# Performance work log

Hardware: AMD Instinct MI355X
Metric: run time of the kernel (lower is better)

The kernel has to match this reference:

```python
import jax, jax.numpy as jnp
import numpy as np

HEADS = 8
DIM_HEAD = 64
DIM = 512
INNER = HEADS * DIM_HEAD  # 512
SCALE = DIM_HEAD ** -0.5


def setup_inputs() -> dict:
    key = jax.random.key(0)
    k1, k2, k3, k4 = jax.random.split(key, 4)
    B, N = 2, 4096
    x = jax.random.normal(k1, (B, N, DIM), dtype=jnp.float32)
    # nn.Linear(dim, inner*3, bias=False): weight [3*inner, dim]; y = x @ W.T
    w_qkv = jax.random.normal(k2, (3 * INNER, DIM), dtype=jnp.float32) * (DIM ** -0.5)
    w_out = jax.random.normal(k3, (DIM, INNER), dtype=jnp.float32) * (INNER ** -0.5)
    b_out = jax.random.normal(k4, (DIM,), dtype=jnp.float32) * 0.01
    return {"x": x, "w_qkv": w_qkv, "w_out": w_out, "b_out": b_out, "H": 64, "W": 64}


def reference(x, w_qkv, w_out, b_out, H, W):
    B, N, _ = x.shape
    qkv = jnp.einsum('bnd,ed->bne', x, w_qkv)  # [B, N, 3*inner]
    q, k, v = jnp.split(qkv, 3, axis=-1)
    def to_heads(t):
        return t.reshape(B, N, HEADS, DIM_HEAD).transpose(0, 2, 1, 3)  # b h n d
    q, k, v = to_heads(q), to_heads(k), to_heads(v)
    dots = jnp.einsum('bhid,bhjd->bhij', q, k) * SCALE
    attn = jax.nn.softmax(dots, axis=-1)  # dropout p=0.0 -> identity
    out = jnp.einsum('bhij,bhjd->bhid', attn, v)
    out = out.transpose(0, 2, 1, 3).reshape(B, N, INNER)
    return jnp.einsum('bne,de->bnd', out, w_out) + b_out
```

## Files before the change

### kernel.cpp

```cpp
#include <hip/hip_runtime.h>
#include <hip/hip_bf16.h>

typedef __hip_bfloat16 bf16;
typedef __attribute__((ext_vector_type(8))) short short8;
typedef __attribute__((ext_vector_type(4))) short shortx4;
typedef __attribute__((ext_vector_type(4))) float floatx4;
typedef __attribute__((ext_vector_type(4))) int intx4;

#define MFMA16(a, b, c) __builtin_amdgcn_mfma_f32_16x16x32_bf16((a), (b), (c), 0, 0, 0)
#define EXP2(x) __builtin_amdgcn_exp2f(x)

__device__ __forceinline__ short f2s(float v) {
    return __builtin_bit_cast(short, __float2bfloat16(v));
}

__device__ __forceinline__ int packhi(float lo, float hi) {
    return (int)__builtin_amdgcn_perm(__builtin_bit_cast(unsigned, hi),
                                      __builtin_bit_cast(unsigned, lo),
                                      0x07060302u);
}

__device__ __forceinline__ short8 cvt8v(float4 f0, float4 f1) {
    short8 r;
    r[0] = f2s(f0.x); r[1] = f2s(f0.y); r[2] = f2s(f0.z); r[3] = f2s(f0.w);
    r[4] = f2s(f1.x); r[5] = f2s(f1.y); r[6] = f2s(f1.z); r[7] = f2s(f1.w);
    return r;
}

__device__ __forceinline__ int swz(int row, int chunk) {
    return row * 64 + ((chunk ^ (row & 7)) << 3);
}
__device__ __forceinline__ int swzv(int row, int chunk) {
    return row * 128 + ((chunk ^ (row & 7)) << 3);
}

__global__ __launch_bounds__(256) void cvt_inputs(
    const float* __restrict__ x, const float* __restrict__ wq,
    const float* __restrict__ wo, bf16* __restrict__ xb,
    bf16* __restrict__ wqb, bf16* __restrict__ wob)
{
    int idx = blockIdx.x * 256 + threadIdx.x;
    const float* src;
    bf16* dst;
    int off;
    if (idx < 524288)      { src = x;  dst = xb;  off = idx; }
    else if (idx < 622592) { src = wq; dst = wqb; off = idx - 524288; }
    else                   { src = wo; dst = wob; off = idx - 622592; }
    float4 f0 = ((const float4*)src)[off * 2];
    float4 f1 = ((const float4*)src)[off * 2 + 1];
    *(short8*)&((short*)dst)[off * 8] = cvt8v(f0, f1);
}

__global__ __launch_bounds__(256) void qkv_gemm(
    const bf16* __restrict__ xb, const bf16* __restrict__ wqb,
    bf16* __restrict__ q, bf16* __restrict__ k, bf16* __restrict__ vt)
{
    __shared__ short pool[20480];
    short (*As)[128][40] = (short(*)[128][40])pool;
    short (*Bs)[128][40] = (short(*)[128][40])(pool + 10240);
    short (*Qt)[144] = (short(*)[144])pool;
    short (*Vt)[136] = (short(*)[136])pool;
    const int t = threadIdx.x;
    const int bm = blockIdx.x * 128;
    const int be = blockIdx.y * 128;
    const int w = t >> 6, lane = t & 63, lq = lane >> 4, lm = lane & 15;
    const int wr = w >> 1, wc = w & 1;
    const int srow = t >> 1, scol = (t & 1) * 16;
    const float C = 0.18033688011112042f;

    const bf16* xp = &xb[(size_t)(bm + srow) * 512 + scol];
    const bf16* wp = &wqb[(size_t)(be + srow) * 512 + scol];

    intx4 xr[2], wr4[2];
    auto issue = [&](int k0) {
        xr[0] = *(const intx4*)(xp + k0);
        xr[1] = *(const intx4*)(xp + k0 + 8);
        wr4[0] = *(const intx4*)(wp + k0);
        wr4[1] = *(const intx4*)(wp + k0 + 8);
    };
    auto commit = [&](int buf) {
        *(intx4*)&As[buf][srow][scol]     = xr[0];
        *(intx4*)&As[buf][srow][scol + 8] = xr[1];
        *(intx4*)&Bs[buf][srow][scol]     = wr4[0];
        *(intx4*)&Bs[buf][srow][scol + 8] = wr4[1];
    };

    floatx4 acc[4][4];
#pragma unroll
    for (int i = 0; i < 4; ++i)
#pragma unroll
        for (int j = 0; j < 4; ++j) acc[i][j] = {0.f, 0.f, 0.f, 0.f};

    issue(0);
    commit(0);
    __syncthreads();
    int cur = 0;
    for (int k0 = 0; k0 < 512; k0 += 32) {
        const bool more = (k0 + 32) < 512;
        if (more) issue(k0 + 32);
        short8 af[4], bf[4];
#pragma unroll
        for (int mt = 0; mt < 4; ++mt) af[mt] = *(const short8*)&As[cur][wr * 64 + mt * 16 + lm][lq * 8];
#pragma unroll
        for (int nt = 0; nt < 4; ++nt) bf[nt] = *(const short8*)&Bs[cur][wc * 64 + nt * 16 + lm][lq * 8];
#pragma unroll
        for (int mt = 0; mt < 4; ++mt)
#pragma unroll
            for (int nt = 0; nt < 4; ++nt)
                acc[mt][nt] = MFMA16(af[mt], bf[nt], acc[mt][nt]);
        if (more) {
            commit(cur ^ 1);
            __syncthreads();
        }
        cur ^= 1;
    }

    const int which = be >> 9;
    __syncthreads();
    if (which < 2) {
        const float scale = (which == 0) ? C : 1.0f;
#pragma unroll
        for (int nt = 0; nt < 4; ++nt) {
            const int e_loc = wc * 64 + nt * 16 + lm;
#pragma unroll
            for (int mt = 0; mt < 4; ++mt)
#pragma unroll
                for (int r = 0; r < 4; ++r)
                    Qt[wr * 64 + mt * 16 + lq * 4 + r][e_loc] = f2s(acc[mt][nt][r] * scale);
        }
        __syncthreads();
        bf16* dst = (which == 0) ? q : k;
        const int tr = t >> 1, th = t & 1;
        const int grow = bm + tr;
        const int b = grow >> 12, n = grow & 4095;
        const int h = ((be + th * 64) & 511) >> 6;
        bf16* p = dst + ((size_t)(b * 8 + h) * 4096 + n) * 64;
#pragma unroll
        for (int c = 0; c < 8; ++c)
            *(intx4*)&p[c * 8] = *(const intx4*)&Qt[tr][th * 64 + c * 8];
    } else {
#pragma unroll
        for (int nt = 0; nt < 4; ++nt) {
            const int e_loc = wc * 64 + nt * 16 + lm;
#pragma unroll
            for (int mt = 0; mt < 4; ++mt) {
                const int col = wr * 64 + 4 * (mt & 1) + 8 * lq + 32 * (mt >> 1);
                shortx4 v4;
#pragma unroll
                for (int r = 0; r < 4; ++r) v4[r] = f2s(acc[mt][nt][r]);
                *(shortx4*)&Vt[e_loc][col] = v4;
            }
        }
        __syncthreads();
        const int b = bm >> 12, n0 = bm & 4095;
        const int h0 = (be - 1024) >> 6;
        const int row = t >> 1, cb = (t & 1) * 64;
        const int h = h0 + (row >> 6), d = row & 63;
        const size_t gb = ((size_t)(b * 8 + h) * 64 + d) * 4096 + n0 + cb;
#pragma unroll
        for (int c = 0; c < 8; ++c)
            *(intx4*)&vt[gb + c * 8] = *(const intx4*)&Vt[row][cb + c * 8];
    }
}

__global__ __launch_bounds__(256, 2) void flash_attn(
    const bf16* __restrict__ q, const bf16* __restrict__ k,
    const bf16* __restrict__ vt, bf16* __restrict__ out)
{
    __shared__ short pool[40960];
    short* Qs  = pool;
    short* Ks0 = pool + 8192;
    short* Vs0 = pool + 24576;
    const int t = threadIdx.x;
    const int n = blockIdx.x;
    const int L = (n & 7) * 64 + (n >> 3);
    const int i0 = (L & 31) * 128;
    const int bh = L >> 5;
    const int w = t >> 6, lane = t & 63, lq = lane >> 4, lm = lane & 15;
    const int h = w >> 1;
    const int par = w & 1;
    const floatx4 zero4 = {0.f, 0.f, 0.f, 0.f};

    const size_t nbase = (size_t)bh * 4096 * 64;
    const size_t vbase = (size_t)bh * 64 * 4096;
    const int r0 = t >> 3, ch = t & 7;

#pragma unroll
    for (int it = 0; it < 4; ++it) {
        int row = it * 32 + r0;
        *(intx4*)&Qs[swz(row, ch)] =
            *(const intx4*)&q[nbase + (size_t)(i0 + row) * 64 + ch * 8];
    }

    const int kr = t >> 1, kc = (t & 1) * 4;
    const int vr = t >> 2, vc = (t & 3) * 4;
    const bf16* kp0 = &k[nbase + (size_t)kr * 64 + kc * 8];
    const bf16* vp0 = &vt[vbase + (size_t)vr * 4096 + vc * 8];
    int kso[4], vso[4];
#pragma unroll
    for (int c = 0; c < 4; ++c) {
        kso[c] = swz(kr, kc + c);
        vso[c] = swzv(vr, vc + c);
    }

    intx4 kreg[4], vreg[4];
    auto issue = [&](int j0n) {
        const intx4* kp = (const intx4*)(kp0 + (size_t)j0n * 64);
        const intx4* vp = (const intx4*)(vp0 + j0n);
#pragma unroll
        for (int c = 0; c < 4; ++c) { kreg[c] = kp[c]; vreg[c] = vp[c]; }
    };
    auto commit = [&](int buf) {
        short* Kb = Ks0 + buf * 8192;
        short* Vb = Vs0 + buf * 8192;
#pragma unroll
        for (int c = 0; c < 4; ++c) {
            *(intx4*)&Kb[kso[c]] = kreg[c];
            *(intx4*)&Vb[vso[c]] = vreg[c];
        }
    };

    issue(0);
    commit(0);
    __syncthreads();

    short8 aq0[4], aq1[4];
#pragma unroll
    for (int g = 0; g < 4; ++g) {
        const int qrow = h * 64 + g * 16 + lm;
        aq0[g] = *(const short8*)&Qs[swz(qrow, lq)];
        aq1[g] = *(const short8*)&Qs[swz(qrow, 4 + lq)];
    }

    float l_lane[4] = {0.f, 0.f, 0.f, 0.f};
    floatx4 o_acc[4][4];
#pragma unroll
    for (int g = 0; g < 4; ++g)
#pragma unroll
        for (int dt = 0; dt < 4; ++dt) o_acc[g][dt] = zero4;

    const int jtb = par * 4;
    int cur = 0;
    for (int j0 = 0; j0 < 4096; j0 += 128) {
        const bool more = (j0 + 128) < 4096;
        if (more) issue(j0 + 128);
        const short* Kb = Ks0 + cur * 8192;
        const short* Vb = Vs0 + cur * 8192;

        intx4 pkA[4], pkB[4];
#pragma unroll
        for (int q2 = 0; q2 < 4; ++q2) {
            const int krow = (jtb + q2) * 16 + lm;
            short8 bk0 = *(const short8*)&Kb[swz(krow, lq)];
            short8 bk1 = *(const short8*)&Kb[swz(krow, 4 + lq)];
#pragma unroll
            for (int g = 0; g < 4; ++g) {
                floatx4 s4 = MFMA16(bk0, aq0[g], zero4);
                s4 = MFMA16(bk1, aq1[g], s4);
                float e0 = EXP2(s4[0]);
                float e1 = EXP2(s4[1]);
                float e2 = EXP2(s4[2]);
                float e3 = EXP2(s4[3]);
                l_lane[g] += (e0 + e1) + (e2 + e3);
                int p01 = packhi(e0, e1), p23 = packhi(e2, e3);
                if (q2 < 2) { pkA[g][q2 * 2] = p01; pkA[g][q2 * 2 + 1] = p23; }
                else { pkB[g][(q2 - 2) * 2] = p01; pkB[g][(q2 - 2) * 2 + 1] = p23; }
            }
        }

        __builtin_amdgcn_s_setprio(1);
#pragma unroll
        for (int dt = 0; dt < 4; ++dt) {
            const int vrow = dt * 16 + lm;
            short8 av0 = *(const short8*)&Vb[swzv(vrow, par * 8 + lq)];
            short8 av1 = *(const short8*)&Vb[swzv(vrow, par * 8 + 4 + lq)];
#pragma unroll
            for (int g = 0; g < 4; ++g) {
                o_acc[g][dt] = MFMA16(av0, __builtin_bit_cast(short8, pkA[g]), o_acc[g][dt]);
                o_acc[g][dt] = MFMA16(av1, __builtin_bit_cast(short8, pkB[g]), o_acc[g][dt]);
            }
        }
        __builtin_amdgcn_s_setprio(0);

        if (more) {
            commit(cur ^ 1);
            __syncthreads();
        }
        cur ^= 1;
    }

    __syncthreads();
    float* Red = (float*)(pool + 8192);
    float* Lx  = (float*)pool;
    if (par == 1) {
#pragma unroll
        for (int g = 0; g < 4; ++g) {
            Lx[h * 256 + g * 64 + lane] = l_lane[g];
#pragma unroll
            for (int dt = 0; dt < 4; ++dt)
#pragma unroll
                for (int r = 0; r < 4; ++r)
                    Red[h * 4096 + ((g * 4 + dt) * 4 + r) * 64 + lane] = o_acc[g][dt][r];
        }
    }
    __syncthreads();
    if (par == 0) {
        const int b = bh >> 3, hd = bh & 7;
        short* Os = pool + 1024 + h * 1024;
        const int il = lane >> 2, cc = (lane & 3) * 16;
#pragma unroll
        for (int g = 0; g < 4; ++g) {
            float l = l_lane[g] + Lx[h * 256 + g * 64 + lane];
#pragma unroll
            for (int dt = 0; dt < 4; ++dt)
#pragma unroll
                for (int r = 0; r < 4; ++r)
                    o_acc[g][dt][r] += Red[h * 4096 + ((g * 4 + dt) * 4 + r) * 64 + lane];
            l += __shfl_xor(l, 16);
            l += __shfl_xor(l, 32);
            const float inv_l = 1.0f / l;
#pragma unroll
            for (int dt = 0; dt < 4; ++dt)
#pragma unroll
                for (int r = 0; r < 4; ++r)
                    Os[lm * 64 + dt * 16 + lq * 4 + r] = f2s(o_acc[g][dt][r] * inv_l);
            const int i = i0 + h * 64 + g * 16 + il;
            intx4 v0 = *(const intx4*)&Os[il * 64 + cc];
            intx4 v1 = *(const intx4*)&Os[il * 64 + cc + 8];
            *(intx4*)&out[((size_t)b * 4096 + i) * 512 + hd * 64 + cc] = v0;
            *(intx4*)&out[((size_t)b * 4096 + i) * 512 + hd * 64 + cc + 8] = v1;
        }
    }
}

__global__ __launch_bounds__(256) void out_gemm(
    const bf16* __restrict__ a, const bf16* __restrict__ wob,
    const float* __restrict__ bias, float* __restrict__ y)
{
    __shared__ short As[2][128][40];
    __shared__ short Bs[2][64][40];
    const int t = threadIdx.x;
    const int bm = blockIdx.x * 128;
    const int be = blockIdx.y * 64;
    const int w = t >> 6, lane = t & 63, lq = lane >> 4, lm = lane & 15;
    const int wr = w >> 1, wc = w & 1;
    const int srow = t >> 1, scol = (t & 1) * 16;
    const int brow = t >> 2, bcol = (t & 3) * 8;

    const bf16* ap = &a[(size_t)(bm + srow) * 512 + scol];
    const bf16* wp = &wob[(size_t)(be + brow) * 512 + bcol];

    intx4 ar[2], br;
    auto issue = [&](int k0) {
        ar[0] = *(const intx4*)(ap + k0);
        ar[1] = *(const intx4*)(ap + k0 + 8);
        br    = *(const intx4*)(wp + k0);
    };
    auto commit = [&](int buf) {
        *(intx4*)&As[buf][srow][scol]     = ar[0];
        *(intx4*)&As[buf][srow][scol + 8] = ar[1];
        *(intx4*)&Bs[buf][brow][bcol]     = br;
    };

    floatx4 acc[4][2];
#pragma unroll
    for (int i = 0; i < 4; ++i)
#pragma unroll
        for (int j = 0; j < 2; ++j) acc[i][j] = {0.f, 0.f, 0.f, 0.f};

    issue(0);
    commit(0);
    __syncthreads();
    int cur = 0;
    for (int k0 = 0; k0 < 512; k0 += 32) {
        const bool more = (k0 + 32) < 512;
        if (more) issue(k0 + 32);
        short8 af[4], bf[2];
#pragma unroll
        for (int mt = 0; mt < 4; ++mt) af[mt] = *(const short8*)&As[cur][wr * 64 + mt * 16 + lm][lq * 8];
#pragma unroll
        for (int nt = 0; nt < 2; ++nt) bf[nt] = *(const short8*)&Bs[cur][wc * 32 + nt * 16 + lm][lq * 8];
#pragma unroll
        for (int mt = 0; mt < 4; ++mt)
#pragma unroll
            for (int nt = 0; nt < 2; ++nt)
                acc[mt][nt] = MFMA16(af[mt], bf[nt], acc[mt][nt]);
        if (more) {
            commit(cur ^ 1);
            __syncthreads();
        }
        cur ^= 1;
    }

#pragma unroll
    for (int nt = 0; nt < 2; ++nt) {
        const int gcol = be + wc * 32 + nt * 16 + lm;
        const float bv = bias[gcol];
#pragma unroll
        for (int mt = 0; mt < 4; ++mt) {
#pragma unroll
            for (int r = 0; r < 4; ++r) {
                int grow = bm + wr * 64 + mt * 16 + lq * 4 + r;
                y[(size_t)grow * 512 + gcol] = acc[mt][nt][r] + bv;
            }
        }
    }
}

extern "C" void kernel_launch(void* const* d_in, const int* in_sizes, int n_in,
                              void* d_out, int out_size, void* d_ws, size_t ws_size,
                              hipStream_t stream) {
    const float* x     = (const float*)d_in[0];
    const float* w_qkv = (const float*)d_in[1];
    const float* w_out = (const float*)d_in[2];
    const float* b_out = (const float*)d_in[3];

    const size_t HEAD_ELEMS = (size_t)16 * 4096 * 64;
    bf16* qw  = (bf16*)d_ws;
    bf16* kw  = qw + HEAD_ELEMS;
    bf16* vtw = kw + HEAD_ELEMS;
    bf16* aw  = vtw + HEAD_ELEMS;
    bf16* xb  = aw + HEAD_ELEMS;
    bf16* wqb = xb + (size_t)8192 * 512;
    bf16* wob = wqb + (size_t)1536 * 512;
    float* y  = (float*)d_out;

    cvt_inputs<<<2560, 256, 0, stream>>>(x, w_qkv, w_out, xb, wqb, wob);
    qkv_gemm<<<dim3(64, 12), 256, 0, stream>>>(xb, wqb, qw, kw, vtw);
    flash_attn<<<dim3(512), 256, 0, stream>>>(qw, kw, vtw, aw);
    out_gemm<<<dim3(64, 8), 256, 0, stream>>>(aw, wob, b_out, y);
}
```

Baseline: 188.9 us.

## Use direct global-to-LDS loads with swizzled tiles and XCD-aware block mapping in GEMMs

New measurement: 187.3 us, median of 2. Within noise of the previous version (-0.9%).

```diff
diff --git a/kernel.cpp b/kernel.cpp
--- a/kernel.cpp
+++ b/kernel.cpp
@@ -32,6 +32,16 @@
 }
 __device__ __forceinline__ int swzv(int row, int chunk) {
     return row * 128 + ((chunk ^ (row & 7)) << 3);
+}
+__device__ __forceinline__ int sfun(int r) { return (r + (r >> 2)) & 3; }
+__device__ __forceinline__ int swz4(int row, int chunk) {
+    return row * 32 + ((chunk ^ sfun(row)) << 3);
+}
+
+__device__ __forceinline__ void gload16(const bf16* g, short* l) {
+    __builtin_amdgcn_global_load_lds(
+        (const __attribute__((address_space(1))) void*)g,
+        (__attribute__((address_space(3))) void*)l, 16, 0, 0);
 }
 
 __global__ __launch_bounds__(256) void cvt_inputs(
@@ -56,34 +66,36 @@
     bf16* __restrict__ q, bf16* __restrict__ k, bf16* __restrict__ vt)
 {
     __shared__ short pool[20480];
-    short (*As)[128][40] = (short(*)[128][40])pool;
-    short (*Bs)[128][40] = (short(*)[128][40])(pool + 10240);
+    short* As = pool;
+    short* Bs = pool + 8192;
     short (*Qt)[144] = (short(*)[144])pool;
     short (*Vt)[136] = (short(*)[136])pool;
     const int t = threadIdx.x;
-    const int bm = blockIdx.x * 128;
-    const int be = blockIdx.y * 128;
+    const int n = blockIdx.x;
+    const int xcd = n & 7, m = n >> 3;
+    const int by = m % 12, bxl = m / 12;
+    const int bm = (xcd * 8 + bxl) * 128;
+    const int be = by * 128;
     const int w = t >> 6, lane = t & 63, lq = lane >> 4, lm = lane & 15;
     const int wr = w >> 1, wc = w & 1;
-    const int srow = t >> 1, scol = (t & 1) * 16;
     const float C = 0.18033688011112042f;
 
-    const bf16* xp = &xb[(size_t)(bm + srow) * 512 + scol];
-    const bf16* wp = &wqb[(size_t)(be + srow) * 512 + scol];
-
-    intx4 xr[2], wr4[2];
-    auto issue = [&](int k0) {
-        xr[0] = *(const intx4*)(xp + k0);
-        xr[1] = *(const intx4*)(xp + k0 + 8);
-        wr4[0] = *(const intx4*)(wp + k0);
-        wr4[1] = *(const intx4*)(wp + k0 + 8);
+    const int r0s = t >> 2, c0s = t & 3;
+    const int ga0 = (c0s ^ sfun(r0s)) * 8;
+    const int ga1 = (c0s ^ sfun(64 + r0s)) * 8;
+    const bf16* xp0 = &xb[(size_t)(bm + r0s) * 512 + ga0];
+    const bf16* xp1 = &xb[(size_t)(bm + 64 + r0s) * 512 + ga1];
+    const bf16* wp0 = &wqb[(size_t)(be + r0s) * 512 + ga0];
+    const bf16* wp1 = &wqb[(size_t)(be + 64 + r0s) * 512 + ga1];
+
+    auto stage = [&](int k0, int buf) {
+        short* Ab = As + buf * 4096;
+        short* Bb = Bs + buf * 4096;
+        gload16(xp0 + k0, &Ab[t * 8]);
+        gload16(xp1 + k0, &Ab[2048 + t * 8]);
+        gload16(wp0 + k0, &Bb[t * 8]);
+        gload16(wp1 + k0, &Bb[2048 + t * 8]);
     };
-    auto commit = [&](int buf) {
-        *(intx4*)&As[buf][srow][scol]     = xr[0];
-        *(intx4*)&As[buf][srow][scol + 8] = xr[1];
-        *(intx4*)&Bs[buf][srow][scol]     = wr4[0];
-        *(intx4*)&Bs[buf][srow][scol + 8] = wr4[1];
-    };
 
     floatx4 acc[4][4];
 #pragma unroll
@@ -91,32 +103,31 @@
 #pragma unroll
         for (int j = 0; j < 4; ++j) acc[i][j] = {0.f, 0.f, 0.f, 0.f};
 
-    issue(0);
-    commit(0);
+    stage(0, 0);
     __syncthreads();
     int cur = 0;
     for (int k0 = 0; k0 < 512; k0 += 32) {
         const bool more = (k0 + 32) < 512;
-        if (more) issue(k0 + 32);
+        if (more) stage(k0 + 32, cur ^ 1);
+        const short* Ab = As + cur * 4096;
+        const short* Bb = Bs + cur * 4096;
         short8 af[4], bf[4];
 #pragma unroll
-        for (int mt = 0; mt < 4; ++mt) af[mt] = *(const short8*)&As[cur][wr * 64 + mt * 16 + lm][lq * 8];
-#pragma unroll
-        for (int nt = 0; nt < 4; ++nt) bf[nt] = *(const short8*)&Bs[cur][wc * 64 + nt * 16 + lm][lq * 8];
+        for (int mt = 0; mt < 4; ++mt)
+            af[mt] = *(const short8*)&Ab[swz4(wr * 64 + mt * 16 + lm, lq)];
+#pragma unroll
+        for (int nt = 0; nt < 4; ++nt)
+            bf[nt] = *(const short8*)&Bb[swz4(wc * 64 + nt * 16 + lm, lq)];
 #pragma unroll
         for (int mt = 0; mt < 4; ++mt)
 #pragma unroll
             for (int nt = 0; nt < 4; ++nt)
                 acc[mt][nt] = MFMA16(af[mt], bf[nt], acc[mt][nt]);
-        if (more) {
-            commit(cur ^ 1);
-            __syncthreads();
-        }
+        __syncthreads();
         cur ^= 1;
     }
 
     const int which = be >> 9;
-    __syncthreads();
     if (which < 2) {
         const float scale = (which == 0) ? C : 1.0f;
 #pragma unroll
@@ -132,9 +143,9 @@
         bf16* dst = (which == 0) ? q : k;
         const int tr = t >> 1, th = t & 1;
         const int grow = bm + tr;
-        const int b = grow >> 12, n = grow & 4095;
+        const int b = grow >> 12, nn = grow & 4095;
         const int h = ((be + th * 64) & 511) >> 6;
-        bf16* p = dst + ((size_t)(b * 8 + h) * 4096 + n) * 64;
+        bf16* p = dst + ((size_t)(b * 8 + h) * 4096 + nn) * 64;
 #pragma unroll
         for (int c = 0; c < 8; ++c)
             *(intx4*)&p[c * 8] = *(const intx4*)&Qt[tr][th * 64 + c * 8];
@@ -337,30 +348,32 @@
     const bf16* __restrict__ a, const bf16* __restrict__ wob,
     const float* __restrict__ bias, float* __restrict__ y)
 {
-    __shared__ short As[2][128][40];
-    __shared__ short Bs[2][64][40];
+    __shared__ short pool[12288];
+    short* As = pool;
+    short* Bs = pool + 8192;
     const int t = threadIdx.x;
-    const int bm = blockIdx.x * 128;
-    const int be = blockIdx.y * 64;
+    const int n = blockIdx.x;
+    const int xcd = n & 7, m = n >> 3;
+    const int by = m & 7, bxl = m >> 3;
+    const int bm = (xcd * 8 + bxl) * 128;
+    const int be = by * 64;
     const int w = t >> 6, lane = t & 63, lq = lane >> 4, lm = lane & 15;
     const int wr = w >> 1, wc = w & 1;
-    const int srow = t >> 1, scol = (t & 1) * 16;
-    const int brow = t >> 2, bcol = (t & 3) * 8;
-
-    const bf16* ap = &a[(size_t)(bm + srow) * 512 + scol];
-    const bf16* wp = &wob[(size_t)(be + brow) * 512 + bcol];
-
-    intx4 ar[2], br;
-    auto issue = [&](int k0) {
-        ar[0] = *(const intx4*)(ap + k0);
-        ar[1] = *(const intx4*)(ap + k0 + 8);
-        br    = *(const intx4*)(wp + k0);
+
+    const int r0s = t >> 2, c0s = t & 3;
+    const int ga0 = (c0s ^ sfun(r0s)) * 8;
+    const int ga1 = (c0s ^ sfun(64 + r0s)) * 8;
+    const bf16* ap0 = &a[(size_t)(bm + r0s) * 512 + ga0];
+    const bf16* ap1 = &a[(size_t)(bm + 64 + r0s) * 512 + ga1];
+    const bf16* wp0 = &wob[(size_t)(be + r0s) * 512 + ga0];
+
+    auto stage = [&](int k0, int buf) {
+        short* Ab = As + buf * 4096;
+        short* Bb = Bs + buf * 2048;
+        gload16(ap0 + k0, &Ab[t * 8]);
+        gload16(ap1 + k0, &Ab[2048 + t * 8]);
+        gload16(wp0 + k0, &Bb[t * 8]);
     };
-    auto commit = [&](int buf) {
-        *(intx4*)&As[buf][srow][scol]     = ar[0];
-        *(intx4*)&As[buf][srow][scol + 8] = ar[1];
-        *(intx4*)&Bs[buf][brow][bcol]     = br;
-    };
 
     floatx4 acc[4][2];
 #pragma unroll
@@ -368,27 +381,27 @@
 #pragma unroll
         for (int j = 0; j < 2; ++j) acc[i][j] = {0.f, 0.f, 0.f, 0.f};
 
-    issue(0);
-    commit(0);
+    stage(0, 0);
     __syncthreads();
     int cur = 0;
     for (int k0 = 0; k0 < 512; k0 += 32) {
         const bool more = (k0 + 32) < 512;
-        if (more) issue(k0 + 32);
+        if (more) stage(k0 + 32, cur ^ 1);
+        const short* Ab = As + cur * 4096;
+        const short* Bb = Bs + cur * 2048;
         short8 af[4], bf[2];
 #pragma unroll
-        for (int mt = 0; mt < 4; ++mt) af[mt] = *(const short8*)&As[cur][wr * 64 + mt * 16 + lm][lq * 8];
-#pragma unroll
-        for (int nt = 0; nt < 2; ++nt) bf[nt] = *(const short8*)&Bs[cur][wc * 32 + nt * 16 + lm][lq * 8];
+        for (int mt = 0; mt < 4; ++mt)
+            af[mt] = *(const short8*)&Ab[swz4(wr * 64 + mt * 16 + lm, lq)];
+#pragma unroll
+        for (int nt = 0; nt < 2; ++nt)
+            bf[nt] = *(const short8*)&Bb[swz4(wc * 32 + nt * 16 + lm, lq)];
 #pragma unroll
         for (int mt = 0; mt < 4; ++mt)
 #pragma unroll
             for (int nt = 0; nt < 2; ++nt)
                 acc[mt][nt] = MFMA16(af[mt], bf[nt], acc[mt][nt]);
-        if (more) {
-            commit(cur ^ 1);
-            __syncthreads();
-        }
+        __syncthreads();
         cur ^= 1;
     }
 
@@ -426,7 +439,7 @@
     float* y  = (float*)d_out;
 
     cvt_inputs<<<2560, 256, 0, stream>>>(x, w_qkv, w_out, xb, wqb, wob);
-    qkv_gemm<<<dim3(64, 12), 256, 0, stream>>>(xb, wqb, qw, kw, vtw);
+    qkv_gemm<<<768, 256, 0, stream>>>(xb, wqb, qw, kw, vtw);
     flash_attn<<<dim3(512), 256, 0, stream>>>(qw, kw, vtw, aw);
-    out_gemm<<<dim3(64, 8), 256, 0, stream>>>(aw, wob, b_out, y);
-}
+    out_gemm<<<512, 256, 0, stream>>>(aw, wob, b_out, y);
+}
```
